# Optimization experiments

Measured on AMD Instinct MI355X. Metric: run time of the kernel, lower is better.

The kernel has to match this reference:

```python
import jax, jax.numpy as jnp
import numpy as np

BS, DIM = 8192, 768
TEMPERATURE = 1.0
EPS = 1e-8


def setup_inputs() -> dict:
    key = jax.random.key(0)
    k1, k2 = jax.random.split(key)
    text_emb = jax.random.normal(k1, (BS, DIM), dtype=jnp.float32)
    ctr_emb = jax.random.normal(k2, (BS, DIM), dtype=jnp.float32)
    return {"text_emb": text_emb, "ctr_emb": ctr_emb}


def _l2norm(x):
    # cosine scorer normalization
    return x / jnp.maximum(jnp.linalg.norm(x, axis=-1, keepdims=True), EPS)


def reference(text_emb, ctr_emb):
    t = _l2norm(text_emb)          # [bs, d]
    c = _l2norm(ctr_emb)           # [bs, d]
    # S[i, j] = cos(text_i, ctr_j) / T  -- single GEMM instead of (bs,bs,d) broadcast
    S = jnp.einsum('id,jd->ij', t, c) / TEMPERATURE   # [bs, bs]
    sim_ii = jnp.diagonal(S)                           # [bs]
    # loss1_i = lse_j S[i,j] - S[i,i]; loss2_i = lse_j S[j,i] - S[i,i]
    loss = (jax.nn.logsumexp(S, axis=1)
            + jax.nn.logsumexp(S, axis=0)
            - 2.0 * sim_ii)
    return jnp.mean(loss)
```

## Files before the change

kernel.cpp:

```cpp
#include <hip/hip_runtime.h>
#include <hip/hip_bf16.h>

#define BS   8192
#define DIM  768
#define TILE 128
#define BK   128

typedef float f32x4 __attribute__((ext_vector_type(4)));
typedef int   i32x4 __attribute__((ext_vector_type(4)));
typedef int   i32x8 __attribute__((ext_vector_type(8)));

__device__ __forceinline__ void async16(const void* g, void* l) {
    __builtin_amdgcn_global_load_lds(
        (const __attribute__((address_space(1))) unsigned int*)g,
        (__attribute__((address_space(3))) unsigned int*)l,
        16, 0, 0);
}

__global__ __launch_bounds__(256) void normalize_kernel(
    const float* __restrict__ text, const float* __restrict__ ctr,
    unsigned char* __restrict__ tq, unsigned char* __restrict__ cq,
    float* __restrict__ sim, float* __restrict__ rowsum, float* __restrict__ colsum) {
    if (blockIdx.x < 64) {
        const int i = blockIdx.x * 256 + threadIdx.x;
        rowsum[i] = 0.f;
        colsum[i] = 0.f;
    }
    const int lane = threadIdx.x & 63;
    const int row  = blockIdx.x * 4 + (threadIdx.x >> 6);
    const size_t base = (size_t)row * DIM;

    float4 t[3], c[3];
    float st = 0.f, sc = 0.f, sd = 0.f;
#pragma unroll
    for (int i = 0; i < 3; ++i) {
        t[i] = *(const float4*)&text[base + lane * 4 + i * 256];
        c[i] = *(const float4*)&ctr [base + lane * 4 + i * 256];
        st += t[i].x*t[i].x + t[i].y*t[i].y + t[i].z*t[i].z + t[i].w*t[i].w;
        sc += c[i].x*c[i].x + c[i].y*c[i].y + c[i].z*c[i].z + c[i].w*c[i].w;
        sd += t[i].x*c[i].x + t[i].y*c[i].y + t[i].z*c[i].z + t[i].w*c[i].w;
    }
#pragma unroll
    for (int off = 1; off < 64; off <<= 1) {
        st += __shfl_xor(st, off);
        sc += __shfl_xor(sc, off);
        sd += __shfl_xor(sd, off);
    }
    const float invt = 1.0f / fmaxf(sqrtf(st), 1e-8f);
    const float invc = 1.0f / fmaxf(sqrtf(sc), 1e-8f);
#pragma unroll
    for (int i = 0; i < 3; ++i) {
        unsigned int wt = (unsigned int)__builtin_amdgcn_cvt_pk_fp8_f32(t[i].x * invt, t[i].y * invt, 0, false);
        wt = (unsigned int)__builtin_amdgcn_cvt_pk_fp8_f32(t[i].z * invt, t[i].w * invt, (int)wt, true);
        unsigned int wcq = (unsigned int)__builtin_amdgcn_cvt_pk_fp8_f32(c[i].x * invc, c[i].y * invc, 0, false);
        wcq = (unsigned int)__builtin_amdgcn_cvt_pk_fp8_f32(c[i].z * invc, c[i].w * invc, (int)wcq, true);
        *(unsigned int*)&tq[base + lane * 4 + i * 256] = wt;
        *(unsigned int*)&cq[base + lane * 4 + i * 256] = wcq;
    }
    if (lane == 0) sim[row] = sd * invt * invc;
}

__global__ __launch_bounds__(256, 3) void gemm_lse_kernel(
    const unsigned char* __restrict__ tq, const unsigned char* __restrict__ cq,
    float* __restrict__ rowsum, float* __restrict__ colsum) {
    __shared__ char ldsA[TILE * BK];
    __shared__ char ldsB[TILE * BK];

    const int tid = threadIdx.x;

    const int bid = blockIdx.x;
    const int xcd = bid & 7, idx = bid >> 3;
    const int tileCol = idx >> 3, rowInBand = idx & 7;
    const int rowBase = (xcd * 8 + rowInBand) * TILE;
    const int colBase = tileCol * TILE;

    const int wave = tid >> 6, lane = tid & 63;
    const int wr = wave >> 1, wc = wave & 1;
    const int quad = lane >> 4, l16 = lane & 15;

    int goff[4], p16[4];
#pragma unroll
    for (int i = 0; i < 4; ++i) {
        const int p  = tid + i * 256;
        const int kc = p >> 8;
        const int row = (p >> 1) & 127;
        const int hl  = (p & 1) ^ (kc & 1);
        goff[i] = row * DIM + kc * 32 + hl * 16;
        p16[i]  = p * 16;
    }
    const unsigned char* gA = tq + (size_t)rowBase * DIM;
    const unsigned char* gB = cq + (size_t)colBase * DIM;

    const int sw = quad & 1;
    int aoff[4], boff[4];
#pragma unroll
    for (int mt = 0; mt < 4; ++mt) aoff[mt] = quad * 4096 + (wr * 64 + mt * 16 + l16) * 32;
#pragma unroll
    for (int nt = 0; nt < 4; ++nt) boff[nt] = quad * 4096 + (wc * 64 + nt * 16 + l16) * 32;

    f32x4 acc[4][4];
#pragma unroll
    for (int mt = 0; mt < 4; ++mt)
#pragma unroll
        for (int nt = 0; nt < 4; ++nt)
            acc[mt][nt] = (f32x4){0.f, 0.f, 0.f, 0.f};

    for (int t = 0; t < 6; ++t) {
        const int k0 = t * BK;
#pragma unroll
        for (int i = 0; i < 4; ++i) {
            async16(gA + goff[i] + k0, ldsA + p16[i]);
            async16(gB + goff[i] + k0, ldsB + p16[i]);
        }
        __syncthreads();

        i32x8 bf[4];
#pragma unroll
        for (int nt = 0; nt < 4; ++nt) {
            i32x4 lo = *(const i32x4*)(ldsB + boff[nt] + sw * 16);
            i32x4 hi = *(const i32x4*)(ldsB + boff[nt] + (sw ^ 1) * 16);
            bf[nt] = __builtin_shufflevector(lo, hi, 0, 1, 2, 3, 4, 5, 6, 7);
        }
#pragma unroll
        for (int mt = 0; mt < 4; ++mt) {
            i32x4 lo = *(const i32x4*)(ldsA + aoff[mt] + sw * 16);
            i32x4 hi = *(const i32x4*)(ldsA + aoff[mt] + (sw ^ 1) * 16);
            i32x8 af = __builtin_shufflevector(lo, hi, 0, 1, 2, 3, 4, 5, 6, 7);
#pragma unroll
            for (int nt = 0; nt < 4; ++nt)
                acc[mt][nt] = __builtin_amdgcn_mfma_scale_f32_16x16x128_f8f6f4(
                    af, bf[nt], acc[mt][nt], 0, 0, 0, 127, 0, 127);
        }
        __syncthreads();
    }

    float rp[4][4];
    float cp[4];
#pragma unroll
    for (int mt = 0; mt < 4; ++mt)
#pragma unroll
        for (int r = 0; r < 4; ++r) rp[mt][r] = 0.f;
#pragma unroll
    for (int nt = 0; nt < 4; ++nt) cp[nt] = 0.f;

#pragma unroll
    for (int mt = 0; mt < 4; ++mt)
#pragma unroll
        for (int nt = 0; nt < 4; ++nt)
#pragma unroll
            for (int r = 0; r < 4; ++r) {
                const float e = __expf(acc[mt][nt][r]);
                rp[mt][r] += e;
                cp[nt]    += e;
            }

#pragma unroll
    for (int mt = 0; mt < 4; ++mt)
#pragma unroll
        for (int r = 0; r < 4; ++r) {
            float v = rp[mt][r];
            v += __shfl_xor(v, 1);
            v += __shfl_xor(v, 2);
            v += __shfl_xor(v, 4);
            v += __shfl_xor(v, 8);
            rp[mt][r] = v;
        }
    if (l16 == 0) {
#pragma unroll
        for (int mt = 0; mt < 4; ++mt)
#pragma unroll
            for (int r = 0; r < 4; ++r)
                atomicAdd(&rowsum[rowBase + wr * 64 + mt * 16 + quad * 4 + r], rp[mt][r]);
    }
#pragma unroll
    for (int nt = 0; nt < 4; ++nt) {
        float v = cp[nt];
        v += __shfl_xor(v, 16);
        v += __shfl_xor(v, 32);
        if (quad == 0)
            atomicAdd(&colsum[colBase + wc * 64 + nt * 16 + l16], v);
    }
}

__global__ __launch_bounds__(1024) void finalize_kernel(
    const float* __restrict__ rowsum, const float* __restrict__ colsum,
    const float* __restrict__ sim, float* __restrict__ out) {
    const int tid = threadIdx.x;
    float acc = 0.f;
#pragma unroll
    for (int i = 0; i < 2; ++i) {
        const int j = (tid + i * 1024) * 4;
        float4 rs = *(const float4*)&rowsum[j];
        float4 cs = *(const float4*)&colsum[j];
        float4 sm = *(const float4*)&sim[j];
        acc += __logf(rs.x) + __logf(rs.y) + __logf(rs.z) + __logf(rs.w);
        acc += __logf(cs.x) + __logf(cs.y) + __logf(cs.z) + __logf(cs.w);
        acc -= 2.f * (sm.x + sm.y + sm.z + sm.w);
    }
#pragma unroll
    for (int off = 1; off < 64; off <<= 1) acc += __shfl_xor(acc, off);
    __shared__ float red[16];
    const int wave = tid >> 6, lane = tid & 63;
    if (lane == 0) red[wave] = acc;
    __syncthreads();
    if (tid == 0) {
        float s = 0.f;
#pragma unroll
        for (int w = 0; w < 16; ++w) s += red[w];
        out[0] = s / (float)BS;
    }
}

extern "C" void kernel_launch(void* const* d_in, const int* in_sizes, int n_in,
                              void* d_out, int out_size, void* d_ws, size_t ws_size,
                              hipStream_t stream) {
    const float* text = (const float*)d_in[0];
    const float* ctr  = (const float*)d_in[1];

    char* ws = (char*)d_ws;
    const size_t embBytes = (size_t)BS * DIM;
    unsigned char* tq = (unsigned char*)ws;
    unsigned char* cq = (unsigned char*)(ws + embBytes);
    float* sim    = (float*)(ws + 2 * embBytes);
    float* rowsum = (float*)(ws + 2 * embBytes + BS * sizeof(float));
    float* colsum = (float*)(ws + 2 * embBytes + 2 * BS * sizeof(float));

    normalize_kernel<<<BS / 4, 256, 0, stream>>>(text, ctr, tq, cq, sim, rowsum, colsum);

    gemm_lse_kernel<<<(BS / TILE) * (BS / TILE), 256, 0, stream>>>(tq, cq, rowsum, colsum);

    finalize_kernel<<<1, 1024, 0, stream>>>(rowsum, colsum, sim, (float*)d_out);
}
```

Measured before the change: 187.1 us.

## Use 256x256 tiles with double-buffered LDS and interleaved MFMA scheduling

Enlarges the GEMM block tile from 128x128 to 256x256 with 512 threads (8 waves, each computing 128x64). LDS is double-buffered so the next K-slice's async global-to-LDS loads are issued in chunks between MFMA groups, with manual waitcnts, sched barriers and setprio. The aim is to raise arithmetic intensity per byte loaded and overlap memory traffic with matrix math. In exchange it uses 128KB of LDS per block and more accumulator registers, which lowers occupancy and leaves fewer blocks (1024) to balance across CUs.

```diff
diff --git a/kernel.cpp b/kernel.cpp
--- a/kernel.cpp
+++ b/kernel.cpp
@@ -3,7 +3,7 @@
 
 #define BS   8192
 #define DIM  768
-#define TILE 128
+#define BM   256
 #define BK   128
 
 typedef float f32x4 __attribute__((ext_vector_type(4)));
@@ -60,30 +60,30 @@
     if (lane == 0) sim[row] = sd * invt * invc;
 }
 
-__global__ __launch_bounds__(256, 3) void gemm_lse_kernel(
+__global__ __launch_bounds__(512, 2) void gemm_lse_kernel(
     const unsigned char* __restrict__ tq, const unsigned char* __restrict__ cq,
     float* __restrict__ rowsum, float* __restrict__ colsum) {
-    __shared__ char ldsA[TILE * BK];
-    __shared__ char ldsB[TILE * BK];
+    __shared__ char ldsA[2][BM * BK];
+    __shared__ char ldsB[2][BM * BK];
 
     const int tid = threadIdx.x;
 
     const int bid = blockIdx.x;
     const int xcd = bid & 7, idx = bid >> 3;
-    const int tileCol = idx >> 3, rowInBand = idx & 7;
-    const int rowBase = (xcd * 8 + rowInBand) * TILE;
-    const int colBase = tileCol * TILE;
+    const int tileCol = idx >> 2, rowInBand = idx & 3;
+    const int rowBase = (xcd * 4 + rowInBand) * BM;
+    const int colBase = tileCol * BM;
 
     const int wave = tid >> 6, lane = tid & 63;
-    const int wr = wave >> 1, wc = wave & 1;
+    const int wr = wave >> 2, wc = wave & 3;
     const int quad = lane >> 4, l16 = lane & 15;
 
     int goff[4], p16[4];
 #pragma unroll
     for (int i = 0; i < 4; ++i) {
-        const int p  = tid + i * 256;
-        const int kc = p >> 8;
-        const int row = (p >> 1) & 127;
+        const int p  = tid + i * 512;
+        const int kc = p >> 9;
+        const int row = (p >> 1) & 255;
         const int hl  = (p & 1) ^ (kc & 1);
         goff[i] = row * DIM + kc * 32 + hl * 16;
         p16[i]  = p * 16;
@@ -91,60 +91,123 @@
     const unsigned char* gA = tq + (size_t)rowBase * DIM;
     const unsigned char* gB = cq + (size_t)colBase * DIM;
 
+#define STAGE(buf, t, i)                                            \
+    do {                                                            \
+        async16(gA + goff[i] + (t) * BK, &ldsA[buf][p16[i]]);       \
+        async16(gB + goff[i] + (t) * BK, &ldsB[buf][p16[i]]);       \
+    } while (0)
+
     const int sw = quad & 1;
-    int aoff[4], boff[4];
-#pragma unroll
-    for (int mt = 0; mt < 4; ++mt) aoff[mt] = quad * 4096 + (wr * 64 + mt * 16 + l16) * 32;
-#pragma unroll
-    for (int nt = 0; nt < 4; ++nt) boff[nt] = quad * 4096 + (wc * 64 + nt * 16 + l16) * 32;
-
-    f32x4 acc[4][4];
-#pragma unroll
-    for (int mt = 0; mt < 4; ++mt)
+    int aoff[8], boff[4];
+#pragma unroll
+    for (int mt = 0; mt < 8; ++mt) aoff[mt] = quad * 8192 + (wr * 128 + mt * 16 + l16) * 32;
+#pragma unroll
+    for (int nt = 0; nt < 4; ++nt) boff[nt] = quad * 8192 + (wc * 64 + nt * 16 + l16) * 32;
+
+#define RD_A(dst, mt, buf)                                                     \
+    do {                                                                       \
+        i32x4 lo = *(const i32x4*)(ldsA[buf] + aoff[mt] + sw * 16);            \
+        i32x4 hi = *(const i32x4*)(ldsA[buf] + aoff[mt] + (sw ^ 1) * 16);      \
+        dst = __builtin_shufflevector(lo, hi, 0, 1, 2, 3, 4, 5, 6, 7);         \
+    } while (0)
+#define RD_B(dst, nt, buf)                                                     \
+    do {                                                                       \
+        i32x4 lo = *(const i32x4*)(ldsB[buf] + boff[nt] + sw * 16);            \
+        i32x4 hi = *(const i32x4*)(ldsB[buf] + boff[nt] + (sw ^ 1) * 16);      \
+        dst = __builtin_shufflevector(lo, hi, 0, 1, 2, 3, 4, 5, 6, 7);         \
+    } while (0)
+#define MFMA8(a0, a1, m0, m1)                                                  \
+    do {                                                                       \
+        acc[m0][0] = __builtin_amdgcn_mfma_scale_f32_16x16x128_f8f6f4(a0, bf0, acc[m0][0], 0, 0, 0, 127, 0, 127); \
+        acc[m0][1] = __builtin_amdgcn_mfma_scale_f32_16x16x128_f8f6f4(a0, bf1, acc[m0][1], 0, 0, 0, 127, 0, 127); \
+        acc[m0][2] = __builtin_amdgcn_mfma_scale_f32_16x16x128_f8f6f4(a0, bf2, acc[m0][2], 0, 0, 0, 127, 0, 127); \
+        acc[m0][3] = __builtin_amdgcn_mfma_scale_f32_16x16x128_f8f6f4(a0, bf3, acc[m0][3], 0, 0, 0, 127, 0, 127); \
+        acc[m1][0] = __builtin_amdgcn_mfma_scale_f32_16x16x128_f8f6f4(a1, bf0, acc[m1][0], 0, 0, 0, 127, 0, 127); \
+        acc[m1][1] = __builtin_amdgcn_mfma_scale_f32_16x16x128_f8f6f4(a1, bf1, acc[m1][1], 0, 0, 0, 127, 0, 127); \
+        acc[m1][2] = __builtin_amdgcn_mfma_scale_f32_16x16x128_f8f6f4(a1, bf2, acc[m1][2], 0, 0, 0, 127, 0, 127); \
+        acc[m1][3] = __builtin_amdgcn_mfma_scale_f32_16x16x128_f8f6f4(a1, bf3, acc[m1][3], 0, 0, 0, 127, 0, 127); \
+    } while (0)
+#define SBAR()  __builtin_amdgcn_sched_barrier(0)
+
+    f32x4 acc[8][4];
+#pragma unroll
+    for (int mt = 0; mt < 8; ++mt)
 #pragma unroll
         for (int nt = 0; nt < 4; ++nt)
             acc[mt][nt] = (f32x4){0.f, 0.f, 0.f, 0.f};
 
+    STAGE(0, 0, 0); STAGE(0, 0, 1); STAGE(0, 0, 2); STAGE(0, 0, 3);
+    SBAR();
+    STAGE(1, 1, 0);
+    SBAR();
+    asm volatile("s_waitcnt vmcnt(2)" ::: "memory");
+    SBAR();
+    __builtin_amdgcn_s_barrier();
+
+#pragma unroll
     for (int t = 0; t < 6; ++t) {
-        const int k0 = t * BK;
-#pragma unroll
-        for (int i = 0; i < 4; ++i) {
-            async16(gA + goff[i] + k0, ldsA + p16[i]);
-            async16(gB + goff[i] + k0, ldsB + p16[i]);
+        const int cur = t & 1;
+        i32x8 bf0, bf1, bf2, bf3, aE0, aE1, aO0, aO1;
+
+        RD_B(bf0, 0, cur); RD_B(bf1, 1, cur); RD_B(bf2, 2, cur); RD_B(bf3, 3, cur);
+        RD_A(aE0, 0, cur); RD_A(aE1, 1, cur);
+
+        RD_A(aO0, 2, cur); RD_A(aO1, 3, cur);
+        if (t < 5) STAGE(cur ^ 1, t + 1, 1);
+        asm volatile("s_waitcnt lgkmcnt(4)" ::: "memory");
+        SBAR();
+        __builtin_amdgcn_s_setprio(1);
+        MFMA8(aE0, aE1, 0, 1);
+        __builtin_amdgcn_s_setprio(0);
+
+        RD_A(aE0, 4, cur); RD_A(aE1, 5, cur);
+        if (t < 5) STAGE(cur ^ 1, t + 1, 2);
+        asm volatile("s_waitcnt lgkmcnt(4)" ::: "memory");
+        SBAR();
+        __builtin_amdgcn_s_setprio(1);
+        MFMA8(aO0, aO1, 2, 3);
+        __builtin_amdgcn_s_setprio(0);
+
+        RD_A(aO0, 6, cur); RD_A(aO1, 7, cur);
+        if (t < 5) STAGE(cur ^ 1, t + 1, 3);
+        asm volatile("s_waitcnt lgkmcnt(4)" ::: "memory");
+        SBAR();
+        __builtin_amdgcn_s_setprio(1);
+        MFMA8(aE0, aE1, 4, 5);
+        __builtin_amdgcn_s_setprio(0);
+
+        asm volatile("s_waitcnt lgkmcnt(0)" ::: "memory");
+        SBAR();
+        __builtin_amdgcn_s_setprio(1);
+        MFMA8(aO0, aO1, 6, 7);
+        __builtin_amdgcn_s_setprio(0);
+
+        if (t < 5) {
+            __builtin_amdgcn_s_barrier();
+            SBAR();
+            if (t < 4) {
+                STAGE(cur, t + 2, 0);
+                SBAR();
+                asm volatile("s_waitcnt vmcnt(2)" ::: "memory");
+            } else {
+                asm volatile("s_waitcnt vmcnt(0)" ::: "memory");
+            }
+            SBAR();
+            __builtin_amdgcn_s_barrier();
         }
-        __syncthreads();
-
-        i32x8 bf[4];
-#pragma unroll
-        for (int nt = 0; nt < 4; ++nt) {
-            i32x4 lo = *(const i32x4*)(ldsB + boff[nt] + sw * 16);
-            i32x4 hi = *(const i32x4*)(ldsB + boff[nt] + (sw ^ 1) * 16);
-            bf[nt] = __builtin_shufflevector(lo, hi, 0, 1, 2, 3, 4, 5, 6, 7);
-        }
-#pragma unroll
-        for (int mt = 0; mt < 4; ++mt) {
-            i32x4 lo = *(const i32x4*)(ldsA + aoff[mt] + sw * 16);
-            i32x4 hi = *(const i32x4*)(ldsA + aoff[mt] + (sw ^ 1) * 16);
-            i32x8 af = __builtin_shufflevector(lo, hi, 0, 1, 2, 3, 4, 5, 6, 7);
-#pragma unroll
-            for (int nt = 0; nt < 4; ++nt)
-                acc[mt][nt] = __builtin_amdgcn_mfma_scale_f32_16x16x128_f8f6f4(
-                    af, bf[nt], acc[mt][nt], 0, 0, 0, 127, 0, 127);
-        }
-        __syncthreads();
-    }
-
-    float rp[4][4];
+    }
+
+    float rp[8][4];
     float cp[4];
 #pragma unroll
-    for (int mt = 0; mt < 4; ++mt)
+    for (int mt = 0; mt < 8; ++mt)
 #pragma unroll
         for (int r = 0; r < 4; ++r) rp[mt][r] = 0.f;
 #pragma unroll
     for (int nt = 0; nt < 4; ++nt) cp[nt] = 0.f;
 
 #pragma unroll
-    for (int mt = 0; mt < 4; ++mt)
+    for (int mt = 0; mt < 8; ++mt)
 #pragma unroll
         for (int nt = 0; nt < 4; ++nt)
 #pragma unroll
@@ -155,7 +218,7 @@
             }
 
 #pragma unroll
-    for (int mt = 0; mt < 4; ++mt)
+    for (int mt = 0; mt < 8; ++mt)
 #pragma unroll
         for (int r = 0; r < 4; ++r) {
             float v = rp[mt][r];
@@ -167,10 +230,10 @@
         }
     if (l16 == 0) {
 #pragma unroll
-        for (int mt = 0; mt < 4; ++mt)
+        for (int mt = 0; mt < 8; ++mt)
 #pragma unroll
             for (int r = 0; r < 4; ++r)
-                atomicAdd(&rowsum[rowBase + wr * 64 + mt * 16 + quad * 4 + r], rp[mt][r]);
+                atomicAdd(&rowsum[rowBase + wr * 128 + mt * 16 + quad * 4 + r], rp[mt][r]);
     }
 #pragma unroll
     for (int nt = 0; nt < 4; ++nt) {
@@ -227,7 +290,7 @@
 
     normalize_kernel<<<BS / 4, 256, 0, stream>>>(text, ctr, tq, cq, sim, rowsum, colsum);
 
-    gemm_lse_kernel<<<(BS / TILE) * (BS / TILE), 256, 0, stream>>>(tq, cq, rowsum, colsum);
+    gemm_lse_kernel<<<(BS / BM) * (BS / BM), 512, 0, stream>>>(tq, cq, rowsum, colsum);
 
     finalize_kernel<<<1, 1024, 0, stream>>>(rowsum, colsum, sim, (float*)d_out);
 }
```

Measured after the change: 169.9 us (median of 4 runs). -9.2%, faster.
